# Optimization experiments

Measured on AMD Instinct MI355X. Metric: run time of the kernel, lower is better.

Reference implementation:

```python
import jax, jax.numpy as jnp
import numpy as np

B, L, H, NH = 32, 512, 256, 4
DH = H // NH
EPS = 1e-12


def setup_inputs() -> dict:
    key = jax.random.key(0)
    ks = jax.random.split(key, 24)
    p = lambda k, shape: 0.02 * jax.random.normal(k, shape, dtype=jnp.float32)
    return {
        "input_tensor": jax.random.normal(ks[0], (B, L, H), dtype=jnp.float32),
        # sorted positive timestamps (seconds-like scale)
        "time_seq": jnp.sort(jax.random.uniform(ks[1], (B, L), dtype=jnp.float32) * 100.0, axis=-1),
        "attention_mask": jnp.zeros((B, 1, L, L), dtype=jnp.float32),
        "item_seq_len": jnp.clip(jax.random.randint(ks[2], (B,), 0, L), 2, L),
        "Wq": p(ks[3], (H, H)), "bq": jnp.zeros((H,), jnp.float32),
        "Wk": p(ks[4], (H, H)), "bk": jnp.zeros((H,), jnp.float32),
        "Wv": p(ks[5], (H, H)), "bv": jnp.zeros((H,), jnp.float32),
        "Wd": p(ks[6], (H, H)), "bd": jnp.zeros((H,), jnp.float32),
        "ln_g": jnp.ones((H,), jnp.float32), "ln_b": jnp.zeros((H,), jnp.float32),
        "Wtq": p(ks[7], (H, H)), "btq": jnp.zeros((H,), jnp.float32),
        "tw1": p(ks[8], (L, L)), "tb1": p(ks[9], (L, L)),
        "tow1": p(ks[10], (L, L)), "tow2": p(ks[11], (L, L)), "tob": p(ks[12], (L, L)),
        "Wt": p(ks[13], (1, 2 * H)), "bt": jnp.zeros((1,), jnp.float32),
    }


def reference(input_tensor, time_seq, attention_mask, item_seq_len,
              Wq, bq, Wk, bk, Wv, bv, Wd, bd, ln_g, ln_b,
              Wtq, btq, tw1, tb1, tow1, tow2, tob, Wt, bt):
    x = input_tensor  # (B, L, H)

    def heads(t):  # (B,L,H) -> (B,NH,L,DH)
        return t.reshape(B, L, NH, DH).transpose(0, 2, 1, 3)

    q = heads(x @ Wq.T + bq)
    k = heads(x @ Wk.T + bk)
    v = heads(x @ Wv.T + bv)

    scores = jnp.einsum('bhqd,bhkd->bhqk', q, k)  # (B,NH,L,L)

    # --- time decay gate ---
    tq = x @ Wtq.T + btq                                  # (B,L,H)
    time_query_key = jnp.tanh(jnp.einsum('bqh,bkh->bqk', tq, x))  # (B,L,L)
    diff = jnp.abs(time_seq[:, :, None] - time_seq[:, None, :])   # |t_i - t_j|
    decay = jnp.tanh(jnp.log1p(diff) * tw1 + tb1)
    decay_gate = tow1 * decay + tow2 * time_query_key + tob       # (B,L,L)
    time_attn = jax.nn.sigmoid(decay_gate)[:, None, :, :]         # (B,1,L,L)

    scores = scores * time_attn / jnp.sqrt(jnp.float32(DH)) + attention_mask
    probs = jax.nn.softmax(scores, axis=-1)

    ctx = jnp.einsum('bhqk,bhkd->bhqd', probs, v)
    ctx = ctx.transpose(0, 2, 1, 3).reshape(B, L, H)

    hs = ctx @ Wd.T + bd + x
    mu = jnp.mean(hs, axis=-1, keepdims=True)
    var = jnp.var(hs, axis=-1, keepdims=True)
    hs = (hs - mu) / jnp.sqrt(var + EPS) * ln_g + ln_b   # (B,L,H)

    bidx = jnp.arange(B)
    emb1 = hs[bidx, item_seq_len - 1]  # (B,H)
    emb2 = hs[bidx, item_seq_len - 2]  # (B,H)
    pred_intervals = jnp.concatenate([emb1, emb2], axis=1) @ Wt.T + bt  # (B,1)
    return hs, pred_intervals
```

## Files before the change

### kernel.cpp

```cpp
#include <hip/hip_runtime.h>
#include <math.h>

#define Bn 32
#define Ln 512
#define Hn 256
#define NHn 4
#define DHn 64

typedef __attribute__((ext_vector_type(8))) short bf16x8;
typedef __attribute__((ext_vector_type(4))) float f32x4;
typedef unsigned int uint32;

__device__ __forceinline__ short f2b(float f) {
    union { float f; uint32 u; } v; v.f = f;
    uint32 r = (v.u + 0x7FFFu + ((v.u >> 16) & 1u)) >> 16;
    return (short)r;
}
__device__ __forceinline__ float b2f(short h) {
    union { uint32 u; float f; } v; v.u = ((uint32)(unsigned short)h) << 16;
    return v.f;
}
__device__ __forceinline__ float fast_tanh(float x) {
    float e = __expf(2.f * x);
    return 1.f - 2.f * __builtin_amdgcn_rcpf(e + 1.f);
}
__device__ __forceinline__ float fast_sigmoid(float x) {
    return __builtin_amdgcn_rcpf(1.f + __expf(-x));
}

__global__ __launch_bounds__(256) void conv_kernel(
    const float* __restrict__ x,
    const float* __restrict__ Wq, const float* __restrict__ Wk,
    const float* __restrict__ Wv, const float* __restrict__ Wtq,
    const float* __restrict__ Wd,
    short* __restrict__ xb, short* __restrict__ wb)
{
    const size_t NLH = (size_t)Bn * Ln * Hn;
    size_t i4 = ((size_t)blockIdx.x * 256 + threadIdx.x) * 4;
    if (i4 < NLH) {
        float4 v = *(const float4*)(x + i4);
        short4 o; o.x = f2b(v.x); o.y = f2b(v.y); o.z = f2b(v.z); o.w = f2b(v.w);
        *(short4*)(xb + i4) = o;
    } else {
        size_t off = i4 - NLH;
        int w = (int)(off >> 16);
        size_t wi = off & 65535;
        const float* src = (w == 0) ? Wq : (w == 1) ? Wk : (w == 2) ? Wv : (w == 3) ? Wtq : Wd;
        float4 v = *(const float4*)(src + wi);
        short4 o; o.x = f2b(v.x); o.y = f2b(v.y); o.z = f2b(v.z); o.w = f2b(v.w);
        *(short4*)(wb + off) = o;
    }
}

struct Acc { f32x4 t[4]; };

template<int K>
__device__ __forceinline__ void gemm_tile_64(
    const short* __restrict__ A,
    const short* __restrict__ Bm,
    short* As, short* Bs, Acc& acc)
{
    const int tid = threadIdx.x;
    const int lane = tid & 63, w = tid >> 6;
    const int quad = lane >> 4, lm = lane & 15;
    const int srow = tid >> 3;
    const int slot = tid & 7;

    bf16x8 av[2], bv[2];
#pragma unroll
    for (int iss = 0; iss < 2; ++iss) {
        int r = srow + iss * 32;
        av[iss] = *(const bf16x8*)(A + (size_t)r * K + slot * 8);
        bv[iss] = *(const bf16x8*)(Bm + (size_t)r * K + slot * 8);
    }
#pragma unroll
    for (int k0 = 0; k0 < K; k0 += 64) {
        __syncthreads();
#pragma unroll
        for (int iss = 0; iss < 2; ++iss) {
            int r = srow + iss * 32;
            *(bf16x8*)(As + r * 72 + slot * 8) = av[iss];
            *(bf16x8*)(Bs + r * 72 + slot * 8) = bv[iss];
        }
        __syncthreads();
        if (k0 + 64 < K) {
#pragma unroll
            for (int iss = 0; iss < 2; ++iss) {
                int r = srow + iss * 32;
                av[iss] = *(const bf16x8*)(A + (size_t)r * K + k0 + 64 + slot * 8);
                bv[iss] = *(const bf16x8*)(Bm + (size_t)r * K + k0 + 64 + slot * 8);
            }
        }
#pragma unroll
        for (int ks = 0; ks < 2; ++ks) {
            bf16x8 a = *(const bf16x8*)(As + (w * 16 + lm) * 72 + ks * 32 + quad * 8);
#pragma unroll
            for (int kt = 0; kt < 4; ++kt) {
                bf16x8 b = *(const bf16x8*)(Bs + (kt * 16 + lm) * 72 + ks * 32 + quad * 8);
                acc.t[kt] = __builtin_amdgcn_mfma_f32_16x16x32_bf16(a, b, acc.t[kt], 0, 0, 0);
            }
        }
    }
}

__global__ __launch_bounds__(256) void proj_kernel(
    const short* __restrict__ xb, const short* __restrict__ wb,
    const float* __restrict__ bq, const float* __restrict__ bk,
    const float* __restrict__ bv, const float* __restrict__ btq,
    short* __restrict__ qb, short* __restrict__ kb,
    short* __restrict__ vt, short* __restrict__ tqb)
{
    __shared__ short As[64 * 72];
    __shared__ short Bs[64 * 72];
    const int tensor = blockIdx.x >> 2;
    const int ncol0 = (blockIdx.x & 3) * 64;
    const int m0 = blockIdx.y * 64;
    const short* A = xb + (size_t)m0 * Hn;
    const short* Bw = wb + (size_t)tensor * 65536 + (size_t)ncol0 * Hn;
    const float* bias = (tensor == 0) ? bq : (tensor == 1) ? bk : (tensor == 2) ? bv : btq;

    Acc acc;
#pragma unroll
    for (int i = 0; i < 4; ++i) acc.t[i] = (f32x4){0.f, 0.f, 0.f, 0.f};
    gemm_tile_64<Hn>(A, Bw, As, Bs, acc);

    const int lane = threadIdx.x & 63, w = threadIdx.x >> 6;
    const int quad = lane >> 4, lm = lane & 15;

    if (tensor == 2) {
#pragma unroll
        for (int kt = 0; kt < 4; ++kt) {
            int n = ncol0 + kt * 16 + lm;
            float bs = bv[n];
            int h = n >> 6, d = n & 63;
#pragma unroll
            for (int r = 0; r < 4; ++r) {
                int row = m0 + w * 16 + quad * 4 + r;
                int bb = row >> 9, l = row & 511;
                vt[((size_t)(bb * NHn + h) * DHn + d) * Ln + l] = f2b(acc.t[kt][r] + bs);
            }
        }
    } else {
        short* out = (tensor == 0) ? qb : (tensor == 1) ? kb : tqb;
#pragma unroll
        for (int kt = 0; kt < 4; ++kt) {
            int n = ncol0 + kt * 16 + lm;
            float bs = bias[n];
#pragma unroll
            for (int r = 0; r < 4; ++r) {
                int row = m0 + w * 16 + quad * 4 + r;
                out[(size_t)row * Hn + n] = f2b(acc.t[kt][r] + bs);
            }
        }
    }
}

__global__ __launch_bounds__(256) void gate_kernel(
    const short* __restrict__ tqb, const short* __restrict__ xb,
    const float* __restrict__ tseq,
    const float* __restrict__ tw1, const float* __restrict__ tb1,
    const float* __restrict__ tow1, const float* __restrict__ tow2,
    const float* __restrict__ tob,
    short* __restrict__ gateb)
{
    __shared__ short As[64 * 72];
    __shared__ short Bs[64 * 72];
    const int b = blockIdx.z;
    const int m0 = blockIdx.y * 64, n0 = blockIdx.x * 64;
    const short* A = tqb + ((size_t)b * Ln + m0) * Hn;
    const short* Bw = xb + ((size_t)b * Ln + n0) * Hn;

    Acc acc;
#pragma unroll
    for (int i = 0; i < 4; ++i) acc.t[i] = (f32x4){0.f, 0.f, 0.f, 0.f};
    gemm_tile_64<Hn>(A, Bw, As, Bs, acc);

    const int lane = threadIdx.x & 63, w = threadIdx.x >> 6;
    const int quad = lane >> 4, lm = lane & 15;
    const float* ts = tseq + (size_t)b * Ln;
    short* go = gateb + (size_t)b * Ln * Ln;
    float ti[4];
#pragma unroll
    for (int r = 0; r < 4; ++r) ti[r] = ts[m0 + w * 16 + quad * 4 + r];
#pragma unroll
    for (int kt = 0; kt < 4; ++kt) {
        int j = n0 + kt * 16 + lm;
        float tj = ts[j];
#pragma unroll
        for (int r = 0; r < 4; ++r) {
            int i = m0 + w * 16 + quad * 4 + r;
            size_t ij = (size_t)i * Ln + j;
            float lg = __logf(1.f + fabsf(ti[r] - tj));
            float dec = fast_tanh(lg * tw1[ij] + tb1[ij]);
            float tqk = fast_tanh(acc.t[kt][r]);
            float dg = tow1[ij] * dec + tow2[ij] * tqk + tob[ij];
            float g = 0.125f * fast_sigmoid(dg);
            go[ij] = f2b(g);
        }
    }
}

__global__ __launch_bounds__(256) void flash_mfma(
    const short* __restrict__ qb, const short* __restrict__ kb,
    const short* __restrict__ vt, const short* __restrict__ gateb,
    const float* __restrict__ mask, short* __restrict__ ctxb)
{
    __shared__ short Ks[64 * 72];
    __shared__ short Vt[64 * 72];
    __shared__ short Ps[4 * 16 * 72];
    const int q0 = blockIdx.x * 64;
    const int h = blockIdx.y, b = blockIdx.z;
    const int tid = threadIdx.x;
    const int w = tid >> 6, lane = tid & 63;
    const int quad = lane >> 4, lm = lane & 15;
    const int srow = tid >> 3, slot = tid & 7;

    bf16x8 qf0, qf1;
    {
        const short* qrow = qb + ((size_t)(b * Ln + q0 + w * 16 + lm)) * Hn + h * DHn;
        qf0 = *(const bf16x8*)(qrow + quad * 8);
        qf1 = *(const bf16x8*)(qrow + 32 + quad * 8);
    }

    f32x4 o[4];
#pragma unroll
    for (int i = 0; i < 4; ++i) o[i] = (f32x4){0.f, 0.f, 0.f, 0.f};
    float m_run[4] = {-INFINITY, -INFINITY, -INFINITY, -INFINITY};
    float l_run[4] = {0.f, 0.f, 0.f, 0.f};
    const short* gr_base = gateb + (size_t)b * Ln * Ln;
    const float* mk_base = mask + (size_t)b * Ln * Ln;
    const int qrow0 = q0 + w * 16 + quad * 4;
    const short* kbase = kb + ((size_t)(b * Ln)) * Hn + h * DHn;
    const short* vbase = vt + (size_t)(b * NHn + h) * DHn * Ln;

    bf16x8 kr[2], vr[2];
#pragma unroll
    for (int iss = 0; iss < 2; ++iss) {
        int r = srow + iss * 32;
        kr[iss] = *(const bf16x8*)(kbase + (size_t)r * Hn + slot * 8);
        vr[iss] = *(const bf16x8*)(vbase + (size_t)r * Ln + slot * 8);
    }

    for (int k0 = 0; k0 < Ln; k0 += 64) {
        __syncthreads();
#pragma unroll
        for (int iss = 0; iss < 2; ++iss) {
            int r = srow + iss * 32;
            *(bf16x8*)(Ks + r * 72 + slot * 8) = kr[iss];
            *(bf16x8*)(Vt + r * 72 + slot * 8) = vr[iss];
        }
        __syncthreads();
        if (k0 + 64 < Ln) {
#pragma unroll
            for (int iss = 0; iss < 2; ++iss) {
                int r = srow + iss * 32;
                kr[iss] = *(const bf16x8*)(kbase + (size_t)(k0 + 64 + r) * Hn + slot * 8);
                vr[iss] = *(const bf16x8*)(vbase + (size_t)r * Ln + k0 + 64 + slot * 8);
            }
        }

        f32x4 s[4];
#pragma unroll
        for (int kt = 0; kt < 4; ++kt) {
            s[kt] = (f32x4){0.f, 0.f, 0.f, 0.f};
            bf16x8 b0 = *(const bf16x8*)(Ks + (kt * 16 + lm) * 72 + quad * 8);
            s[kt] = __builtin_amdgcn_mfma_f32_16x16x32_bf16(qf0, b0, s[kt], 0, 0, 0);
            bf16x8 b1 = *(const bf16x8*)(Ks + (kt * 16 + lm) * 72 + 32 + quad * 8);
            s[kt] = __builtin_amdgcn_mfma_f32_16x16x32_bf16(qf1, b1, s[kt], 0, 0, 0);
        }

        float mnew[4];
#pragma unroll
        for (int r = 0; r < 4; ++r) mnew[r] = m_run[r];
#pragma unroll
        for (int kt = 0; kt < 4; ++kt) {
            int col = k0 + kt * 16 + lm;
#pragma unroll
            for (int r = 0; r < 4; ++r) {
                float g  = b2f(gr_base[(size_t)(qrow0 + r) * Ln + col]);
                float mv = mk_base[(size_t)(qrow0 + r) * Ln + col];
                float sv = s[kt][r] * g + mv;
                s[kt][r] = sv;
                mnew[r] = fmaxf(mnew[r], sv);
            }
        }
        float alpha[4], rsum[4];
#pragma unroll
        for (int r = 0; r < 4; ++r) {
#pragma unroll
            for (int off = 1; off < 16; off <<= 1)
                mnew[r] = fmaxf(mnew[r], __shfl_xor(mnew[r], off, 64));
            alpha[r] = __expf(m_run[r] - mnew[r]);
            m_run[r] = mnew[r];
            rsum[r] = 0.f;
        }
        float p[4][4];
#pragma unroll
        for (int kt = 0; kt < 4; ++kt)
#pragma unroll
            for (int r = 0; r < 4; ++r) {
                float pv = __expf(s[kt][r] - m_run[r]);
                p[kt][r] = pv;
                rsum[r] += pv;
            }
#pragma unroll
        for (int r = 0; r < 4; ++r) {
#pragma unroll
            for (int off = 1; off < 16; off <<= 1) rsum[r] += __shfl_xor(rsum[r], off, 64);
            l_run[r] = l_run[r] * alpha[r] + rsum[r];
#pragma unroll
            for (int ot = 0; ot < 4; ++ot) o[ot][r] *= alpha[r];
        }
        short* pw = Ps + w * 16 * 72;
#pragma unroll
        for (int kt = 0; kt < 4; ++kt)
#pragma unroll
            for (int r = 0; r < 4; ++r)
                pw[(quad * 4 + r) * 72 + kt * 16 + lm] = f2b(p[kt][r]);

#pragma unroll
        for (int ks = 0; ks < 2; ++ks) {
            bf16x8 pa = *(const bf16x8*)(pw + lm * 72 + ks * 32 + quad * 8);
#pragma unroll
            for (int ot = 0; ot < 4; ++ot) {
                bf16x8 vv = *(const bf16x8*)(Vt + (ot * 16 + lm) * 72 + ks * 32 + quad * 8);
                o[ot] = __builtin_amdgcn_mfma_f32_16x16x32_bf16(pa, vv, o[ot], 0, 0, 0);
            }
        }
    }

    float inv[4];
#pragma unroll
    for (int r = 0; r < 4; ++r) inv[r] = 1.0f / l_run[r];
#pragma unroll
    for (int ot = 0; ot < 4; ++ot) {
        int d = h * DHn + ot * 16 + lm;
#pragma unroll
        for (int r = 0; r < 4; ++r) {
            int row = b * Ln + qrow0 + r;
            ctxb[(size_t)row * Hn + d] = f2b(o[ot][r] * inv[r]);
        }
    }
}

__global__ __launch_bounds__(256) void outproj_ln_kernel(
    const short* __restrict__ ctxb, const short* __restrict__ wdb,
    const float* __restrict__ bd, const float* __restrict__ x,
    const float* __restrict__ g, const float* __restrict__ beta,
    float* __restrict__ out)
{
    __shared__ short As[64 * 264];
    __shared__ short Bs[64 * 72];
    const int m0 = blockIdx.x * 64;
    const int tid = threadIdx.x;
    const int lane = tid & 63, w = tid >> 6;
    const int quad = lane >> 4, lm = lane & 15;
    const int srow = tid >> 3, slot = tid & 7;

#pragma unroll
    for (int iss = 0; iss < 2; ++iss) {
        int r = srow + iss * 32;
#pragma unroll
        for (int c = 0; c < 4; ++c) {
            bf16x8 av = *(const bf16x8*)(ctxb + (size_t)(m0 + r) * Hn + c * 64 + slot * 8);
            *(bf16x8*)(As + r * 264 + c * 64 + slot * 8) = av;
        }
    }

    f32x4 acc[4][4];
#pragma unroll
    for (int i = 0; i < 4; ++i)
#pragma unroll
        for (int j = 0; j < 4; ++j) acc[i][j] = (f32x4){0.f, 0.f, 0.f, 0.f};

    bf16x8 bv[2];
#pragma unroll
    for (int iss = 0; iss < 2; ++iss)
        bv[iss] = *(const bf16x8*)(wdb + (size_t)(srow + iss * 32) * Hn + slot * 8);

#pragma unroll
    for (int nt = 0; nt < 4; ++nt) {
#pragma unroll
        for (int k0 = 0; k0 < Hn; k0 += 64) {
#pragma unroll
            for (int iss = 0; iss < 2; ++iss)
                *(bf16x8*)(Bs + (srow + iss * 32) * 72 + slot * 8) = bv[iss];
            __syncthreads();
            int k1 = (k0 + 64 < Hn) ? k0 + 64 : 0;
            int nt1 = (k0 + 64 < Hn) ? nt : nt + 1;
            if (nt1 < 4) {
                const short* wsrc = wdb + (size_t)(nt1 * 64) * Hn + k1;
#pragma unroll
                for (int iss = 0; iss < 2; ++iss)
                    bv[iss] = *(const bf16x8*)(wsrc + (size_t)(srow + iss * 32) * Hn + slot * 8);
            }
#pragma unroll
            for (int ks = 0; ks < 2; ++ks) {
                bf16x8 a = *(const bf16x8*)(As + (w * 16 + lm) * 264 + k0 + ks * 32 + quad * 8);
#pragma unroll
                for (int kt = 0; kt < 4; ++kt) {
                    bf16x8 bb = *(const bf16x8*)(Bs + (kt * 16 + lm) * 72 + ks * 32 + quad * 8);
                    acc[nt][kt] = __builtin_amdgcn_mfma_f32_16x16x32_bf16(a, bb, acc[nt][kt], 0, 0, 0);
                }
            }
            __syncthreads();
        }
    }

    const int rl0 = w * 16 + quad * 4;
    float s1[4] = {0.f, 0.f, 0.f, 0.f}, s2[4] = {0.f, 0.f, 0.f, 0.f};
#pragma unroll
    for (int nt = 0; nt < 4; ++nt)
#pragma unroll
        for (int kt = 0; kt < 4; ++kt) {
            int col = nt * 64 + kt * 16 + lm;
            float bdv = bd[col];
#pragma unroll
            for (int r = 0; r < 4; ++r) {
                float xv = x[(size_t)(m0 + rl0 + r) * Hn + col];
                float hv = acc[nt][kt][r] + bdv + xv;
                acc[nt][kt][r] = hv;
                s1[r] += hv;
                s2[r] += hv * hv;
            }
        }
#pragma unroll
    for (int r = 0; r < 4; ++r) {
#pragma unroll
        for (int off = 1; off < 16; off <<= 1) {
            s1[r] += __shfl_xor(s1[r], off, 64);
            s2[r] += __shfl_xor(s2[r], off, 64);
        }
    }
    float mu[4], rstd[4];
#pragma unroll
    for (int r = 0; r < 4; ++r) {
        mu[r] = s1[r] * (1.f / 256.f);
        float var = s2[r] * (1.f / 256.f) - mu[r] * mu[r];
        rstd[r] = rsqrtf(var + 1e-12f);
    }
#pragma unroll
    for (int nt = 0; nt < 4; ++nt)
#pragma unroll
        for (int kt = 0; kt < 4; ++kt) {
            int col = nt * 64 + kt * 16 + lm;
            float gv = g[col], bb = beta[col];
#pragma unroll
            for (int r = 0; r < 4; ++r)
                out[(size_t)(m0 + rl0 + r) * Hn + col] =
                    (acc[nt][kt][r] - mu[r]) * rstd[r] * gv + bb;
        }
}

__global__ __launch_bounds__(256) void pred_kernel(const float* __restrict__ hs,
                                                   const int* __restrict__ lens,
                                                   const float* __restrict__ Wt,
                                                   const float* __restrict__ bt,
                                                   float* __restrict__ pred)
{
    const int b = blockIdx.x, t = threadIdx.x;
    int len = lens[b];
    float e1 = hs[((size_t)b * Ln + (len - 1)) * Hn + t];
    float e2 = hs[((size_t)b * Ln + (len - 2)) * Hn + t];
    float v = e1 * Wt[t] + e2 * Wt[Hn + t];
#pragma unroll
    for (int off = 32; off > 0; off >>= 1) v += __shfl_xor(v, off, 64);
    __shared__ float ps[4];
    if ((t & 63) == 0) ps[t >> 6] = v;
    __syncthreads();
    if (t == 0) pred[b] = ps[0] + ps[1] + ps[2] + ps[3] + bt[0];
}

extern "C" void kernel_launch(void* const* d_in, const int* in_sizes, int n_in,
                              void* d_out, int out_size, void* d_ws, size_t ws_size,
                              hipStream_t stream) {
    (void)in_sizes; (void)n_in; (void)out_size; (void)ws_size;
    const float* x    = (const float*)d_in[0];
    const float* tseq = (const float*)d_in[1];
    const float* mask = (const float*)d_in[2];
    const int*   lens = (const int*)d_in[3];
    const float* Wq = (const float*)d_in[4];  const float* bq = (const float*)d_in[5];
    const float* Wk = (const float*)d_in[6];  const float* bk = (const float*)d_in[7];
    const float* Wv = (const float*)d_in[8];  const float* bv = (const float*)d_in[9];
    const float* Wd = (const float*)d_in[10]; const float* bd = (const float*)d_in[11];
    const float* ln_g = (const float*)d_in[12]; const float* ln_b = (const float*)d_in[13];
    const float* Wtq = (const float*)d_in[14]; const float* btq = (const float*)d_in[15];
    const float* tw1 = (const float*)d_in[16]; const float* tb1 = (const float*)d_in[17];
    const float* tow1 = (const float*)d_in[18]; const float* tow2 = (const float*)d_in[19];
    const float* tob = (const float*)d_in[20];
    const float* Wt = (const float*)d_in[21]; const float* bt = (const float*)d_in[22];

    const size_t NLH = (size_t)Bn * Ln * Hn;
    short* ws = (short*)d_ws;
    short* xb    = ws;
    short* wb    = xb + NLH;
    short* qb    = wb + 5 * 65536;
    short* kb    = qb + NLH;
    short* vt    = kb + NLH;
    short* tqb   = vt + NLH;
    short* gateb = tqb + NLH;
    short* ctxb  = tqb;
    float* out   = (float*)d_out;

    dim3 blk(256);
    conv_kernel<<<dim3(4416), blk, 0, stream>>>(x, Wq, Wk, Wv, Wtq, Wd, xb, wb);
    proj_kernel<<<dim3(16, 256), blk, 0, stream>>>(xb, wb, bq, bk, bv, btq, qb, kb, vt, tqb);
    gate_kernel<<<dim3(8, 8, Bn), blk, 0, stream>>>(tqb, xb, tseq, tw1, tb1, tow1, tow2, tob, gateb);
    flash_mfma<<<dim3(8, NHn, Bn), blk, 0, stream>>>(qb, kb, vt, gateb, mask, ctxb);
    outproj_ln_kernel<<<dim3(256), blk, 0, stream>>>(ctxb, wb + 4 * 65536, bd, x, ln_g, ln_b, out);
    pred_kernel<<<dim3(Bn), blk, 0, stream>>>(out, lens, Wt, bt, out + NLH);
}
```

Before: 272.1 us.

## Drop register prefetch, reorder flash grid by head, load Wd directly from global

```diff
diff --git a/kernel.cpp b/kernel.cpp
--- a/kernel.cpp
+++ b/kernel.cpp
@@ -54,11 +54,10 @@
 
 struct Acc { f32x4 t[4]; };
 
-template<int K>
 __device__ __forceinline__ void gemm_tile_64(
     const short* __restrict__ A,
     const short* __restrict__ Bm,
-    short* As, short* Bs, Acc& acc)
+    int K, short* As, short* Bs, Acc& acc)
 {
     const int tid = threadIdx.x;
     const int lane = tid & 63, w = tid >> 6;
@@ -66,31 +65,17 @@
     const int srow = tid >> 3;
     const int slot = tid & 7;
 
-    bf16x8 av[2], bv[2];
-#pragma unroll
-    for (int iss = 0; iss < 2; ++iss) {
-        int r = srow + iss * 32;
-        av[iss] = *(const bf16x8*)(A + (size_t)r * K + slot * 8);
-        bv[iss] = *(const bf16x8*)(Bm + (size_t)r * K + slot * 8);
-    }
-#pragma unroll
     for (int k0 = 0; k0 < K; k0 += 64) {
         __syncthreads();
 #pragma unroll
         for (int iss = 0; iss < 2; ++iss) {
             int r = srow + iss * 32;
-            *(bf16x8*)(As + r * 72 + slot * 8) = av[iss];
-            *(bf16x8*)(Bs + r * 72 + slot * 8) = bv[iss];
+            bf16x8 av = *(const bf16x8*)(A + (size_t)r * K + k0 + slot * 8);
+            bf16x8 bv = *(const bf16x8*)(Bm + (size_t)r * K + k0 + slot * 8);
+            *(bf16x8*)(As + r * 72 + slot * 8) = av;
+            *(bf16x8*)(Bs + r * 72 + slot * 8) = bv;
         }
         __syncthreads();
-        if (k0 + 64 < K) {
-#pragma unroll
-            for (int iss = 0; iss < 2; ++iss) {
-                int r = srow + iss * 32;
-                av[iss] = *(const bf16x8*)(A + (size_t)r * K + k0 + 64 + slot * 8);
-                bv[iss] = *(const bf16x8*)(Bm + (size_t)r * K + k0 + 64 + slot * 8);
-            }
-        }
 #pragma unroll
         for (int ks = 0; ks < 2; ++ks) {
             bf16x8 a = *(const bf16x8*)(As + (w * 16 + lm) * 72 + ks * 32 + quad * 8);
@@ -122,7 +107,7 @@
     Acc acc;
 #pragma unroll
     for (int i = 0; i < 4; ++i) acc.t[i] = (f32x4){0.f, 0.f, 0.f, 0.f};
-    gemm_tile_64<Hn>(A, Bw, As, Bs, acc);
+    gemm_tile_64(A, Bw, Hn, As, Bs, acc);
 
     const int lane = threadIdx.x & 63, w = threadIdx.x >> 6;
     const int quad = lane >> 4, lm = lane & 15;
@@ -173,7 +158,7 @@
     Acc acc;
 #pragma unroll
     for (int i = 0; i < 4; ++i) acc.t[i] = (f32x4){0.f, 0.f, 0.f, 0.f};
-    gemm_tile_64<Hn>(A, Bw, As, Bs, acc);
+    gemm_tile_64(A, Bw, Hn, As, Bs, acc);
 
     const int lane = threadIdx.x & 63, w = threadIdx.x >> 6;
     const int quad = lane >> 4, lm = lane & 15;
@@ -208,8 +193,9 @@
     __shared__ short Ks[64 * 72];
     __shared__ short Vt[64 * 72];
     __shared__ short Ps[4 * 16 * 72];
-    const int q0 = blockIdx.x * 64;
-    const int h = blockIdx.y, b = blockIdx.z;
+    const int h = blockIdx.x;
+    const int q0 = blockIdx.y * 64;
+    const int b = blockIdx.z;
     const int tid = threadIdx.x;
     const int w = tid >> 6, lane = tid & 63;
     const int quad = lane >> 4, lm = lane & 15;
@@ -233,31 +219,17 @@
     const short* kbase = kb + ((size_t)(b * Ln)) * Hn + h * DHn;
     const short* vbase = vt + (size_t)(b * NHn + h) * DHn * Ln;
 
-    bf16x8 kr[2], vr[2];
-#pragma unroll
-    for (int iss = 0; iss < 2; ++iss) {
-        int r = srow + iss * 32;
-        kr[iss] = *(const bf16x8*)(kbase + (size_t)r * Hn + slot * 8);
-        vr[iss] = *(const bf16x8*)(vbase + (size_t)r * Ln + slot * 8);
-    }
-
     for (int k0 = 0; k0 < Ln; k0 += 64) {
         __syncthreads();
 #pragma unroll
         for (int iss = 0; iss < 2; ++iss) {
             int r = srow + iss * 32;
-            *(bf16x8*)(Ks + r * 72 + slot * 8) = kr[iss];
-            *(bf16x8*)(Vt + r * 72 + slot * 8) = vr[iss];
+            bf16x8 kv = *(const bf16x8*)(kbase + (size_t)(k0 + r) * Hn + slot * 8);
+            bf16x8 vv = *(const bf16x8*)(vbase + (size_t)r * Ln + k0 + slot * 8);
+            *(bf16x8*)(Ks + r * 72 + slot * 8) = kv;
+            *(bf16x8*)(Vt + r * 72 + slot * 8) = vv;
         }
         __syncthreads();
-        if (k0 + 64 < Ln) {
-#pragma unroll
-            for (int iss = 0; iss < 2; ++iss) {
-                int r = srow + iss * 32;
-                kr[iss] = *(const bf16x8*)(kbase + (size_t)(k0 + 64 + r) * Hn + slot * 8);
-                vr[iss] = *(const bf16x8*)(vbase + (size_t)r * Ln + k0 + 64 + slot * 8);
-            }
-        }
 
         f32x4 s[4];
 #pragma unroll
@@ -349,23 +321,16 @@
     const float* __restrict__ g, const float* __restrict__ beta,
     float* __restrict__ out)
 {
-    __shared__ short As[64 * 264];
-    __shared__ short Bs[64 * 72];
     const int m0 = blockIdx.x * 64;
     const int tid = threadIdx.x;
     const int lane = tid & 63, w = tid >> 6;
     const int quad = lane >> 4, lm = lane & 15;
-    const int srow = tid >> 3, slot = tid & 7;
-
-#pragma unroll
-    for (int iss = 0; iss < 2; ++iss) {
-        int r = srow + iss * 32;
-#pragma unroll
-        for (int c = 0; c < 4; ++c) {
-            bf16x8 av = *(const bf16x8*)(ctxb + (size_t)(m0 + r) * Hn + c * 64 + slot * 8);
-            *(bf16x8*)(As + r * 264 + c * 64 + slot * 8) = av;
-        }
-    }
+
+    const short* arow = ctxb + (size_t)(m0 + w * 16 + lm) * Hn;
+    bf16x8 af[8];
+#pragma unroll
+    for (int k8 = 0; k8 < 8; ++k8)
+        af[k8] = *(const bf16x8*)(arow + k8 * 32 + quad * 8);
 
     f32x4 acc[4][4];
 #pragma unroll
@@ -373,38 +338,15 @@
 #pragma unroll
         for (int j = 0; j < 4; ++j) acc[i][j] = (f32x4){0.f, 0.f, 0.f, 0.f};
 
-    bf16x8 bv[2];
-#pragma unroll
-    for (int iss = 0; iss < 2; ++iss)
-        bv[iss] = *(const bf16x8*)(wdb + (size_t)(srow + iss * 32) * Hn + slot * 8);
-
-#pragma unroll
-    for (int nt = 0; nt < 4; ++nt) {
-#pragma unroll
-        for (int k0 = 0; k0 < Hn; k0 += 64) {
-#pragma unroll
-            for (int iss = 0; iss < 2; ++iss)
-                *(bf16x8*)(Bs + (srow + iss * 32) * 72 + slot * 8) = bv[iss];
-            __syncthreads();
-            int k1 = (k0 + 64 < Hn) ? k0 + 64 : 0;
-            int nt1 = (k0 + 64 < Hn) ? nt : nt + 1;
-            if (nt1 < 4) {
-                const short* wsrc = wdb + (size_t)(nt1 * 64) * Hn + k1;
-#pragma unroll
-                for (int iss = 0; iss < 2; ++iss)
-                    bv[iss] = *(const bf16x8*)(wsrc + (size_t)(srow + iss * 32) * Hn + slot * 8);
-            }
-#pragma unroll
-            for (int ks = 0; ks < 2; ++ks) {
-                bf16x8 a = *(const bf16x8*)(As + (w * 16 + lm) * 264 + k0 + ks * 32 + quad * 8);
-#pragma unroll
-                for (int kt = 0; kt < 4; ++kt) {
-                    bf16x8 bb = *(const bf16x8*)(Bs + (kt * 16 + lm) * 72 + ks * 32 + quad * 8);
-                    acc[nt][kt] = __builtin_amdgcn_mfma_f32_16x16x32_bf16(a, bb, acc[nt][kt], 0, 0, 0);
-                }
-            }
-            __syncthreads();
-        }
+#pragma unroll
+    for (int k8 = 0; k8 < 8; ++k8) {
+#pragma unroll
+        for (int nt = 0; nt < 4; ++nt)
+#pragma unroll
+            for (int kt = 0; kt < 4; ++kt) {
+                bf16x8 bf = *(const bf16x8*)(wdb + (size_t)(nt * 64 + kt * 16 + lm) * Hn + k8 * 32 + quad * 8);
+                acc[nt][kt] = __builtin_amdgcn_mfma_f32_16x16x32_bf16(af[k8], bf, acc[nt][kt], 0, 0, 0);
+            }
     }
 
     const int rl0 = w * 16 + quad * 4;
@@ -506,7 +448,7 @@
     conv_kernel<<<dim3(4416), blk, 0, stream>>>(x, Wq, Wk, Wv, Wtq, Wd, xb, wb);
     proj_kernel<<<dim3(16, 256), blk, 0, stream>>>(xb, wb, bq, bk, bv, btq, qb, kb, vt, tqb);
     gate_kernel<<<dim3(8, 8, Bn), blk, 0, stream>>>(tqb, xb, tseq, tw1, tb1, tow1, tow2, tob, gateb);
-    flash_mfma<<<dim3(8, NHn, Bn), blk, 0, stream>>>(qb, kb, vt, gateb, mask, ctxb);
+    flash_mfma<<<dim3(NHn, 8, Bn), blk, 0, stream>>>(qb, kb, vt, gateb, mask, ctxb);
     outproj_ln_kernel<<<dim3(256), blk, 0, stream>>>(ctxb, wb + 4 * 65536, bd, x, ln_g, ln_b, out);
     pred_kernel<<<dim3(Bn), blk, 0, stream>>>(out, lens, Wt, bt, out + NLH);
 }
```

Measured after the change: 234.9 us. -13.7%, faster.
